# Kernel tuning notes

Hardware: AMD Instinct MI355X
Metric: run time of the kernel (lower is better)

## Reference

```python
import jax, jax.numpy as jnp
import numpy as np

EPS = 1e-5

def sage_conv(x, edge_index, w_l, b_l, w_r):
    # PyG SAGEConv with mean aggregation: lin_l(mean of source-neighbor feats per dst) + lin_r(x)
    n = x.shape[0]
    src, dst = edge_index[0], edge_index[1]
    agg = jax.ops.segment_sum(x[src], dst, num_segments=n)  # [N, d]
    deg = jax.ops.segment_sum(jnp.ones((edge_index.shape[1],), x.dtype), dst, num_segments=n)
    agg = agg / jnp.maximum(deg, 1.0)[:, None]
    return agg @ w_l + b_l + x @ w_r

def batchnorm_eval(x, gamma, beta, mean, var):
    return (x - mean) * (gamma * jax.lax.rsqrt(var + EPS)) + beta

def setup_inputs() -> dict:
    key = jax.random.key(0)
    ks = jax.random.split(key, 12)
    N, E, D, H, O = 10000, 160000, 512, 512, 256
    inp = {
        'x': jax.random.normal(ks[0], (N, D), jnp.float32),
        'edge_index': jax.random.randint(ks[1], (2, E), 0, N, jnp.int32),
        'w_l1': jax.random.normal(ks[2], (D, H), jnp.float32) * (1.0 / np.sqrt(D)),
        'b1': jnp.zeros((H,), jnp.float32),
        'w_r1': jax.random.normal(ks[3], (D, H), jnp.float32) * (1.0 / np.sqrt(D)),
        'bn1_gamma': jnp.ones((H,), jnp.float32),
        'bn1_beta': jnp.zeros((H,), jnp.float32),
        'bn1_mean': jax.random.normal(ks[4], (H,), jnp.float32) * 0.1,
        'bn1_var': jax.random.uniform(ks[5], (H,), jnp.float32, 0.5, 1.5),
        'w_l2': jax.random.normal(ks[6], (H, H), jnp.float32) * (1.0 / np.sqrt(H)),
        'b2': jnp.zeros((H,), jnp.float32),
        'w_r2': jax.random.normal(ks[7], (H, H), jnp.float32) * (1.0 / np.sqrt(H)),
        'bn2_gamma': jnp.ones((H,), jnp.float32),
        'bn2_beta': jnp.zeros((H,), jnp.float32),
        'bn2_mean': jax.random.normal(ks[8], (H,), jnp.float32) * 0.1,
        'bn2_var': jax.random.uniform(ks[9], (H,), jnp.float32, 0.5, 1.5),
        'w_l3': jax.random.normal(ks[10], (H, O), jnp.float32) * (1.0 / np.sqrt(H)),
        'b3': jnp.zeros((O,), jnp.float32),
        'w_r3': jax.random.normal(ks[11], (H, O), jnp.float32) * (1.0 / np.sqrt(H)),
    }
    return inp

def reference(x, edge_index, w_l1, b1, w_r1, bn1_gamma, bn1_beta, bn1_mean, bn1_var,
              w_l2, b2, w_r2, bn2_gamma, bn2_beta, bn2_mean, bn2_var,
              w_l3, b3, w_r3):
    # Layer 1: SAGEConv -> BN (eval) -> ReLU (dropout is identity in eval)
    h = sage_conv(x, edge_index, w_l1, b1, w_r1)
    h = jax.nn.relu(batchnorm_eval(h, bn1_gamma, bn1_beta, bn1_mean, bn1_var))
    # Layer 2
    h = sage_conv(h, edge_index, w_l2, b2, w_r2)
    h = jax.nn.relu(batchnorm_eval(h, bn2_gamma, bn2_beta, bn2_mean, bn2_var))
    # Layer 3 (no BN/ReLU)
    return sage_conv(h, edge_index, w_l3, b3, w_r3)
```

## Files before the change

### kernel.cpp

```cpp
#include <hip/hip_runtime.h>

#define NNODE 10000
#define NEDGE 160000
#define SLOTS 128

using frag8 = __attribute__((ext_vector_type(8))) short;
using f32x4 = __attribute__((ext_vector_type(4))) float;

__device__ __forceinline__ unsigned short f2bf(float f) {
    union { float f; unsigned u; } v; v.f = f;
    unsigned r = (v.u + 0x7fffu + ((v.u >> 16) & 1u)) >> 16;
    return (unsigned short)r;
}
__device__ __forceinline__ float bf2f(unsigned short s) {
    union { unsigned u; float f; } v; v.u = ((unsigned)s) << 16; return v.f;
}

__global__ void k_fillp(const int* __restrict__ src, const int* __restrict__ dst,
                        int E, int* __restrict__ cnt, int* __restrict__ csrp) {
    int e = blockIdx.x * 256 + threadIdx.x;
    if (e < E) {
        int d = dst[e];
        int p = atomicAdd(&cnt[d], 1);
        csrp[(long)d * SLOTS + p] = src[e];
    }
}

__global__ __launch_bounds__(256) void k_prep(
    const float* __restrict__ x, unsigned short* __restrict__ xb,
    const float* __restrict__ wl1, const float* __restrict__ wr1,
    const float* __restrict__ wl2, const float* __restrict__ wr2,
    const float* __restrict__ wl3, const float* __restrict__ wr3,
    unsigned short* __restrict__ bt1, unsigned short* __restrict__ bt2,
    unsigned short* __restrict__ bt3,
    const float* __restrict__ b1, const float* __restrict__ g1, const float* __restrict__ be1,
    const float* __restrict__ m1, const float* __restrict__ v1,
    const float* __restrict__ b2, const float* __restrict__ g2, const float* __restrict__ be2,
    const float* __restrict__ m2, const float* __restrict__ v2,
    const float* __restrict__ b3,
    float* __restrict__ sc1, float* __restrict__ sh1,
    float* __restrict__ sc2, float* __restrict__ sh2,
    float* __restrict__ sc3, float* __restrict__ sh3) {
    const int b = blockIdx.x, tid = threadIdx.x;
    if (b < 5000) {
        int i = b * 256 + tid;
        float4 f = ((const float4*)x)[i];
        ushort4 o;
        o.x = f2bf(f.x); o.y = f2bf(f.y); o.z = f2bf(f.z); o.w = f2bf(f.w);
        ((ushort4*)xb)[i] = o;
        return;
    }
    if (b == 6280) {
        for (int t = tid; t < 512; t += 256) {
            float s1 = g1[t] * rsqrtf(v1[t] + 1e-5f);
            sc1[t] = s1; sh1[t] = (b1[t] - m1[t]) * s1 + be1[t];
            float s2 = g2[t] * rsqrtf(v2[t] + 1e-5f);
            sc2[t] = s2; sh2[t] = (b2[t] - m2[t]) * s2 + be2[t];
            sc3[t] = 1.0f; sh3[t] = (t < 256) ? 0.0f : b3[t - 256];
        }
        return;
    }
    __shared__ float t[32][33];
    int tj = b - 5000;
    const float* srcp; unsigned short* dstp; int C, koff, ntilesN, rowoff, dstride;
    if (tj < 1024) {
        int job = tj >> 8; int tile = tj & 255; C = 512; ntilesN = 16;
        srcp = (job == 0) ? wl1 : (job == 1) ? wr1 : (job == 2) ? wl2 : wr2;
        dstp = (job < 2) ? bt1 : bt2; koff = (job & 1) * 512; rowoff = 0; dstride = 1024;
        tj = tile;
    } else {
        int jj = tj - 1024; int job = jj >> 7; int tile = jj & 127; C = 256; ntilesN = 8;
        srcp = (job == 0) ? wl3 : wr3; dstp = bt3; koff = 0; rowoff = job * 256; dstride = 512;
        tj = tile;
    }
    int k0 = (tj / ntilesN) * 32, c0 = (tj % ntilesN) * 32;
    int tx = tid & 31, ty = tid >> 5;
#pragma unroll
    for (int q = 0; q < 4; q++)
        t[ty + 8 * q][tx] = srcp[(long)(k0 + ty + 8 * q) * C + c0 + tx];
    __syncthreads();
#pragma unroll
    for (int q = 0; q < 4; q++)
        dstp[(long)(rowoff + c0 + ty + 8 * q) * dstride + koff + k0 + tx] = f2bf(t[tx][ty + 8 * q]);
}

__global__ __launch_bounds__(64) void k_agg(const unsigned short* __restrict__ S,
                                            const int* __restrict__ cnt, const int* __restrict__ csrp,
                                            unsigned short* __restrict__ outb) {
    const int n = blockIdx.x;
    const int c = threadIdx.x * 8;
    const int e = cnt[n];
    const int* __restrict__ lst = csrp + (long)n * SLOTS;
    float a[8];
#pragma unroll
    for (int k = 0; k < 8; k++) a[k] = 0.f;
    int i = 0;
    for (; i + 4 <= e; i += 4) {
        int r0 = lst[i], r1 = lst[i + 1], r2 = lst[i + 2], r3 = lst[i + 3];
        uint4 u0 = *(const uint4*)(S + (long)r0 * 512 + c);
        uint4 u1 = *(const uint4*)(S + (long)r1 * 512 + c);
        uint4 u2 = *(const uint4*)(S + (long)r2 * 512 + c);
        uint4 u3 = *(const uint4*)(S + (long)r3 * 512 + c);
#define ACC(u) \
        a[0] += bf2f((unsigned short)((u).x & 0xffffu)); a[1] += bf2f((unsigned short)((u).x >> 16)); \
        a[2] += bf2f((unsigned short)((u).y & 0xffffu)); a[3] += bf2f((unsigned short)((u).y >> 16)); \
        a[4] += bf2f((unsigned short)((u).z & 0xffffu)); a[5] += bf2f((unsigned short)((u).z >> 16)); \
        a[6] += bf2f((unsigned short)((u).w & 0xffffu)); a[7] += bf2f((unsigned short)((u).w >> 16));
        ACC(u0) ACC(u1) ACC(u2) ACC(u3)
    }
    for (; i < e; i++) {
        uint4 u = *(const uint4*)(S + (long)lst[i] * 512 + c);
        ACC(u)
    }
#undef ACC
    const float inv = 1.f / (float)(e > 1 ? e : 1);
    uint4 o;
    o.x = (unsigned)f2bf(a[0] * inv) | ((unsigned)f2bf(a[1] * inv) << 16);
    o.y = (unsigned)f2bf(a[2] * inv) | ((unsigned)f2bf(a[3] * inv) << 16);
    o.z = (unsigned)f2bf(a[4] * inv) | ((unsigned)f2bf(a[5] * inv) << 16);
    o.w = (unsigned)f2bf(a[6] * inv) | ((unsigned)f2bf(a[7] * inv) << 16);
    *(uint4*)(outb + (long)n * 512 + c) = o;
}

__global__ __launch_bounds__(64) void k_agg_fuse(const unsigned short* __restrict__ PQ,
                                                 const int* __restrict__ cnt, const int* __restrict__ csrp,
                                                 float* __restrict__ out) {
    const int n = blockIdx.x;
    const int c = threadIdx.x * 4;
    const int e = cnt[n];
    const int* __restrict__ lst = csrp + (long)n * SLOTS;
    uint2 q = *(const uint2*)(PQ + (long)n * 512 + 256 + c);
    float a0 = 0.f, a1 = 0.f, a2 = 0.f, a3 = 0.f;
    int i = 0;
    for (; i + 4 <= e; i += 4) {
        int r0 = lst[i], r1 = lst[i + 1], r2 = lst[i + 2], r3 = lst[i + 3];
        uint2 u0 = *(const uint2*)(PQ + (long)r0 * 512 + c);
        uint2 u1 = *(const uint2*)(PQ + (long)r1 * 512 + c);
        uint2 u2 = *(const uint2*)(PQ + (long)r2 * 512 + c);
        uint2 u3 = *(const uint2*)(PQ + (long)r3 * 512 + c);
#define ACC(u) \
        a0 += bf2f((unsigned short)((u).x & 0xffffu)); a1 += bf2f((unsigned short)((u).x >> 16)); \
        a2 += bf2f((unsigned short)((u).y & 0xffffu)); a3 += bf2f((unsigned short)((u).y >> 16));
        ACC(u0) ACC(u1) ACC(u2) ACC(u3)
    }
    for (; i < e; i++) {
        uint2 u = *(const uint2*)(PQ + (long)lst[i] * 512 + c);
        ACC(u)
    }
#undef ACC
    const float inv = 1.f / (float)(e > 1 ? e : 1);
    float4 o;
    o.x = a0 * inv + bf2f((unsigned short)(q.x & 0xffffu));
    o.y = a1 * inv + bf2f((unsigned short)(q.x >> 16));
    o.z = a2 * inv + bf2f((unsigned short)(q.y & 0xffffu));
    o.w = a3 * inv + bf2f((unsigned short)(q.y >> 16));
    *(float4*)&out[(long)n * 256 + c] = o;
}

template <int MODE, int NOUT, bool SPLIT>
__global__ __launch_bounds__(256, 3) void k_gemm(const unsigned short* __restrict__ Agg,
                                                 const unsigned short* __restrict__ Self,
                                                 const unsigned short* __restrict__ Bt,
                                                 const float* __restrict__ sc, const float* __restrict__ sh,
                                                 unsigned short* __restrict__ hout, int M) {
    constexpr int NT = NOUT / 128;
    constexpr int QSH = (NT == 4) ? 5 : 4;
    constexpr int KSTEPS = SPLIT ? 16 : 8;
    constexpr int BSTR = SPLIT ? 1024 : 512;
    const int b = blockIdx.x;
    const int X = b & 7;
    const int q = (b >> 3) & (NT - 1);
    const int g = b >> QSH;
    const int m0 = (g * 8 + X) * 64;
    if (m0 >= M) return;
    const int n0 = q * 128;

    __shared__ __align__(16) short As[2][64 * 64];
    __shared__ __align__(16) short Bs[2][128 * 64];
    const int tid = threadIdx.x;
    const int w = tid >> 6, lane = tid & 63;
    const int wm = (w >> 1) * 32, wn = (w & 1) * 64;
    const int fr = lane & 15, fq = lane >> 4, sw = fr & 7;
    const int srow = w * 8 + (lane >> 3);
    const int scol = (((lane & 7) ^ (lane >> 3)) * 8);
    const int ldsOff = w * 8 * 64;

    f32x4 acc[2][4];
#pragma unroll
    for (int i = 0; i < 2; i++)
#pragma unroll
        for (int j = 0; j < 4; j++)
#pragma unroll
            for (int r = 0; r < 4; r++) acc[i][j][r] = 0.f;

    auto issue = [&](int t, int buf) {
        const short* abase;
        int kk;
        if constexpr (SPLIT) {
            abase = (const short*)((t < 8) ? Agg : Self);
            kk = (t & 7) * 64;
        } else {
            abase = (const short*)Self;
            kk = t * 64;
        }
        const int k0 = t * 64;
#pragma unroll
        for (int cch = 0; cch < 2; cch++) {
            __builtin_amdgcn_global_load_lds(
                (const __attribute__((address_space(1))) void*)(abase + (long)(m0 + cch * 32 + srow) * 512 + kk + scol),
                (__attribute__((address_space(3))) void*)(&As[buf][ldsOff + cch * 32 * 64]), 16, 0, 0);
        }
#pragma unroll
        for (int cch = 0; cch < 4; cch++) {
            __builtin_amdgcn_global_load_lds(
                (const __attribute__((address_space(1))) void*)((const short*)Bt + (long)(n0 + cch * 32 + srow) * BSTR + k0 + scol),
                (__attribute__((address_space(3))) void*)(&Bs[buf][ldsOff + cch * 32 * 64]), 16, 0, 0);
        }
    };

    issue(0, 0);
#pragma unroll
    for (int t = 0; t < KSTEPS; t++) {
        const int cur = t & 1;
        __syncthreads();
        if (t < KSTEPS - 1) issue(t + 1, cur ^ 1);
#pragma unroll
        for (int ks = 0; ks < 2; ks++) {
            frag8 af[2], bf[4];
#pragma unroll
            for (int i = 0; i < 2; i++)
                af[i] = *(const frag8*)(&As[cur][(wm + i * 16 + fr) * 64 + (((ks * 4 + fq) ^ sw) * 8)]);
#pragma unroll
            for (int j = 0; j < 4; j++)
                bf[j] = *(const frag8*)(&Bs[cur][(wn + j * 16 + fr) * 64 + (((ks * 4 + fq) ^ sw) * 8)]);
#pragma unroll
            for (int i = 0; i < 2; i++)
#pragma unroll
                for (int j = 0; j < 4; j++)
                    acc[i][j] = __builtin_amdgcn_mfma_f32_16x16x32_bf16(bf[j], af[i], acc[i][j], 0, 0, 0);
        }
    }

#pragma unroll
    for (int j = 0; j < 4; j++) {
        const int colb = n0 + wn + j * 16 + fq * 4;
        const float4 s4 = *(const float4*)&sc[colb];
        const float4 h4 = *(const float4*)&sh[colb];
#pragma unroll
        for (int i = 0; i < 2; i++) {
            const int row = m0 + wm + i * 16 + fr;
            if (row < M) {
                float y0 = acc[i][j][0] * s4.x + h4.x;
                float y1 = acc[i][j][1] * s4.y + h4.y;
                float y2 = acc[i][j][2] * s4.z + h4.z;
                float y3 = acc[i][j][3] * s4.w + h4.w;
                if constexpr (MODE == 0) {
                    y0 = fmaxf(y0, 0.f); y1 = fmaxf(y1, 0.f);
                    y2 = fmaxf(y2, 0.f); y3 = fmaxf(y3, 0.f);
                }
                uint2 o;
                o.x = (unsigned)f2bf(y0) | ((unsigned)f2bf(y1) << 16);
                o.y = (unsigned)f2bf(y2) | ((unsigned)f2bf(y3) << 16);
                *(uint2*)&hout[(long)row * NOUT + colb] = o;
            }
        }
    }
}

extern "C" void kernel_launch(void* const* d_in, const int* in_sizes, int n_in,
                              void* d_out, int out_size, void* d_ws, size_t ws_size,
                              hipStream_t stream) {
    const float* x    = (const float*)d_in[0];
    const int*   ei   = (const int*)d_in[1];
    const float* w_l1 = (const float*)d_in[2];
    const float* b1   = (const float*)d_in[3];
    const float* w_r1 = (const float*)d_in[4];
    const float* g1   = (const float*)d_in[5];
    const float* be1  = (const float*)d_in[6];
    const float* m1   = (const float*)d_in[7];
    const float* v1   = (const float*)d_in[8];
    const float* w_l2 = (const float*)d_in[9];
    const float* b2   = (const float*)d_in[10];
    const float* w_r2 = (const float*)d_in[11];
    const float* g2   = (const float*)d_in[12];
    const float* be2  = (const float*)d_in[13];
    const float* m2   = (const float*)d_in[14];
    const float* v2   = (const float*)d_in[15];
    const float* w_l3 = (const float*)d_in[16];
    const float* b3   = (const float*)d_in[17];
    const float* w_r3 = (const float*)d_in[18];
    float* out = (float*)d_out;

    const int N = NNODE, E = NEDGE;
    const int* srcI = ei;
    const int* dstI = ei + E;

    char* w = (char*)d_ws;
    auto alloc = [&](size_t bytes) { void* p = (void*)w; w += (bytes + 255) & ~(size_t)255; return p; };
    int* cnt  = (int*)alloc((size_t)N * 4);
    int* csrp = (int*)alloc((size_t)N * SLOTS * 4);
    unsigned short* xb   = (unsigned short*)alloc((size_t)N * 512 * 2);
    unsigned short* bt1  = (unsigned short*)alloc((size_t)512 * 1024 * 2);
    unsigned short* bt2  = (unsigned short*)alloc((size_t)512 * 1024 * 2);
    unsigned short* bt3  = (unsigned short*)alloc((size_t)512 * 512 * 2);
    float* sc1 = (float*)alloc(512 * 4); float* sh1 = (float*)alloc(512 * 4);
    float* sc2 = (float*)alloc(512 * 4); float* sh2 = (float*)alloc(512 * 4);
    float* sc3 = (float*)alloc(512 * 4); float* sh3 = (float*)alloc(512 * 4);
    unsigned short* agg_a = (unsigned short*)alloc((size_t)N * 512 * 2);
    unsigned short* h1    = (unsigned short*)alloc((size_t)N * 512 * 2);
    unsigned short* h2    = (unsigned short*)alloc((size_t)N * 512 * 2);
    (void)alloc(256 * 1024);

    hipMemsetAsync(cnt, 0, (size_t)N * 4, stream);
    k_prep<<<6281, 256, 0, stream>>>(x, xb, w_l1, w_r1, w_l2, w_r2, w_l3, w_r3,
                                     bt1, bt2, bt3,
                                     b1, g1, be1, m1, v1, b2, g2, be2, m2, v2, b3,
                                     sc1, sh1, sc2, sh2, sc3, sh3);
    k_fillp<<<(E + 255) / 256, 256, 0, stream>>>(srcI, dstI, E, cnt, csrp);

    k_agg<<<N, 64, 0, stream>>>(xb, cnt, csrp, agg_a);
    k_gemm<0, 512, true><<<640, 256, 0, stream>>>(agg_a, xb, bt1, sc1, sh1, h1, N);
    k_agg<<<N, 64, 0, stream>>>(h1, cnt, csrp, agg_a);
    k_gemm<0, 512, true><<<640, 256, 0, stream>>>(agg_a, h1, bt2, sc2, sh2, h2, N);
    k_gemm<2, 512, false><<<640, 256, 0, stream>>>(h2, h2, bt3, sc3, sh3, agg_a, N);
    k_agg_fuse<<<N, 64, 0, stream>>>(agg_a, cnt, csrp, out);
}
```

Before: 224.8 us.

## Overlap neighbor aggregation with self-term GEMM in one mixed kernel

Each layer's GEMM is split into a self term (x @ w_r) and an aggregate term. A combined kernel interleaves aggregation blocks (four nodes per 256-thread block) with self-GEMM blocks, so the two independent workloads run concurrently. The self GEMM writes fp32 partial results to a new workspace buffer, which a second GEMM over the aggregate reads and combines with BN and ReLU in its epilogue. This trades an extra fp32 write and read of N×512 floats per layer for overlap of memory-bound gather work with MFMA work.

```diff
diff --git a/kernel.cpp b/kernel.cpp
--- a/kernel.cpp
+++ b/kernel.cpp
@@ -84,42 +84,315 @@
         dstp[(long)(rowoff + c0 + ty + 8 * q) * dstride + koff + k0 + tx] = f2bf(t[tx][ty + 8 * q]);
 }
 
-__global__ __launch_bounds__(64) void k_agg(const unsigned short* __restrict__ S,
-                                            const int* __restrict__ cnt, const int* __restrict__ csrp,
-                                            unsigned short* __restrict__ outb) {
-    const int n = blockIdx.x;
-    const int c = threadIdx.x * 8;
-    const int e = cnt[n];
-    const int* __restrict__ lst = csrp + (long)n * SLOTS;
-    float a[8];
-#pragma unroll
-    for (int k = 0; k < 8; k++) a[k] = 0.f;
-    int i = 0;
-    for (; i + 4 <= e; i += 4) {
-        int r0 = lst[i], r1 = lst[i + 1], r2 = lst[i + 2], r3 = lst[i + 3];
-        uint4 u0 = *(const uint4*)(S + (long)r0 * 512 + c);
-        uint4 u1 = *(const uint4*)(S + (long)r1 * 512 + c);
-        uint4 u2 = *(const uint4*)(S + (long)r2 * 512 + c);
-        uint4 u3 = *(const uint4*)(S + (long)r3 * 512 + c);
+__global__ __launch_bounds__(256, 3) void k_mixA(
+    const unsigned short* __restrict__ S,
+    const int* __restrict__ cnt, const int* __restrict__ csrp,
+    unsigned short* __restrict__ aggOut,
+    const unsigned short* __restrict__ Bt,
+    float* __restrict__ Qf) {
+    __shared__ __align__(16) short As[2][64 * 64];
+    __shared__ __align__(16) short Bs[2][128 * 64];
+    const int b = blockIdx.x;
+    const int tid = threadIdx.x;
+
+    if ((b % 5) != 4) {
+        const int agg_idx = (b / 5) * 4 + (b % 5);
+        const int n = agg_idx * 4 + (tid >> 6);
+        if (n >= NNODE) return;
+        const int c = (tid & 63) * 8;
+        const int e = cnt[n];
+        const int* __restrict__ lst = csrp + (long)n * SLOTS;
+        float a[8];
+#pragma unroll
+        for (int k = 0; k < 8; k++) a[k] = 0.f;
+        int i = 0;
+        for (; i + 4 <= e; i += 4) {
+            int r0 = lst[i], r1 = lst[i + 1], r2 = lst[i + 2], r3 = lst[i + 3];
+            uint4 u0 = *(const uint4*)(S + (long)r0 * 512 + c);
+            uint4 u1 = *(const uint4*)(S + (long)r1 * 512 + c);
+            uint4 u2 = *(const uint4*)(S + (long)r2 * 512 + c);
+            uint4 u3 = *(const uint4*)(S + (long)r3 * 512 + c);
 #define ACC(u) \
-        a[0] += bf2f((unsigned short)((u).x & 0xffffu)); a[1] += bf2f((unsigned short)((u).x >> 16)); \
-        a[2] += bf2f((unsigned short)((u).y & 0xffffu)); a[3] += bf2f((unsigned short)((u).y >> 16)); \
-        a[4] += bf2f((unsigned short)((u).z & 0xffffu)); a[5] += bf2f((unsigned short)((u).z >> 16)); \
-        a[6] += bf2f((unsigned short)((u).w & 0xffffu)); a[7] += bf2f((unsigned short)((u).w >> 16));
-        ACC(u0) ACC(u1) ACC(u2) ACC(u3)
-    }
-    for (; i < e; i++) {
-        uint4 u = *(const uint4*)(S + (long)lst[i] * 512 + c);
-        ACC(u)
-    }
+            a[0] += bf2f((unsigned short)((u).x & 0xffffu)); a[1] += bf2f((unsigned short)((u).x >> 16)); \
+            a[2] += bf2f((unsigned short)((u).y & 0xffffu)); a[3] += bf2f((unsigned short)((u).y >> 16)); \
+            a[4] += bf2f((unsigned short)((u).z & 0xffffu)); a[5] += bf2f((unsigned short)((u).z >> 16)); \
+            a[6] += bf2f((unsigned short)((u).w & 0xffffu)); a[7] += bf2f((unsigned short)((u).w >> 16));
+            ACC(u0) ACC(u1) ACC(u2) ACC(u3)
+        }
+        for (; i < e; i++) {
+            uint4 u = *(const uint4*)(S + (long)lst[i] * 512 + c);
+            ACC(u)
+        }
 #undef ACC
-    const float inv = 1.f / (float)(e > 1 ? e : 1);
-    uint4 o;
-    o.x = (unsigned)f2bf(a[0] * inv) | ((unsigned)f2bf(a[1] * inv) << 16);
-    o.y = (unsigned)f2bf(a[2] * inv) | ((unsigned)f2bf(a[3] * inv) << 16);
-    o.z = (unsigned)f2bf(a[4] * inv) | ((unsigned)f2bf(a[5] * inv) << 16);
-    o.w = (unsigned)f2bf(a[6] * inv) | ((unsigned)f2bf(a[7] * inv) << 16);
-    *(uint4*)(outb + (long)n * 512 + c) = o;
+        const float inv = 1.f / (float)(e > 1 ? e : 1);
+        uint4 o;
+        o.x = (unsigned)f2bf(a[0] * inv) | ((unsigned)f2bf(a[1] * inv) << 16);
+        o.y = (unsigned)f2bf(a[2] * inv) | ((unsigned)f2bf(a[3] * inv) << 16);
+        o.z = (unsigned)f2bf(a[4] * inv) | ((unsigned)f2bf(a[5] * inv) << 16);
+        o.w = (unsigned)f2bf(a[6] * inv) | ((unsigned)f2bf(a[7] * inv) << 16);
+        *(uint4*)(aggOut + (long)n * 512 + c) = o;
+        return;
+    }
+
+    const int id = b / 5;
+    const int X = id & 7;
+    const int q = (id >> 3) & 3;
+    const int g = id >> 5;
+    const int m0 = (g * 8 + X) * 64;
+    if (m0 >= NNODE) return;
+    const int n0 = q * 128;
+
+    const int w = tid >> 6, lane = tid & 63;
+    const int wm = (w >> 1) * 32, wn = (w & 1) * 64;
+    const int fr = lane & 15, fq = lane >> 4, sw = fr & 7;
+    const int srow = w * 8 + (lane >> 3);
+    const int scol = (((lane & 7) ^ (lane >> 3)) * 8);
+    const int ldsOff = w * 8 * 64;
+
+    f32x4 acc[2][4];
+#pragma unroll
+    for (int i = 0; i < 2; i++)
+#pragma unroll
+        for (int j = 0; j < 4; j++)
+#pragma unroll
+            for (int r = 0; r < 4; r++) acc[i][j][r] = 0.f;
+
+    auto issue = [&](int t, int buf) {
+        const int k0 = t * 64;
+#pragma unroll
+        for (int cch = 0; cch < 2; cch++) {
+            __builtin_amdgcn_global_load_lds(
+                (const __attribute__((address_space(1))) void*)((const short*)S + (long)(m0 + cch * 32 + srow) * 512 + k0 + scol),
+                (__attribute__((address_space(3))) void*)(&As[buf][ldsOff + cch * 32 * 64]), 16, 0, 0);
+        }
+#pragma unroll
+        for (int cch = 0; cch < 4; cch++) {
+            __builtin_amdgcn_global_load_lds(
+                (const __attribute__((address_space(1))) void*)((const short*)Bt + (long)(n0 + cch * 32 + srow) * 1024 + 512 + k0 + scol),
+                (__attribute__((address_space(3))) void*)(&Bs[buf][ldsOff + cch * 32 * 64]), 16, 0, 0);
+        }
+    };
+
+    issue(0, 0);
+#pragma unroll
+    for (int t = 0; t < 8; t++) {
+        const int cur = t & 1;
+        __syncthreads();
+        if (t < 7) issue(t + 1, cur ^ 1);
+#pragma unroll
+        for (int ks = 0; ks < 2; ks++) {
+            frag8 af[2], bf[4];
+#pragma unroll
+            for (int i = 0; i < 2; i++)
+                af[i] = *(const frag8*)(&As[cur][(wm + i * 16 + fr) * 64 + (((ks * 4 + fq) ^ sw) * 8)]);
+#pragma unroll
+            for (int j = 0; j < 4; j++)
+                bf[j] = *(const frag8*)(&Bs[cur][(wn + j * 16 + fr) * 64 + (((ks * 4 + fq) ^ sw) * 8)]);
+#pragma unroll
+            for (int i = 0; i < 2; i++)
+#pragma unroll
+                for (int j = 0; j < 4; j++)
+                    acc[i][j] = __builtin_amdgcn_mfma_f32_16x16x32_bf16(bf[j], af[i], acc[i][j], 0, 0, 0);
+        }
+    }
+
+#pragma unroll
+    for (int j = 0; j < 4; j++) {
+        const int colb = n0 + wn + j * 16 + fq * 4;
+#pragma unroll
+        for (int i = 0; i < 2; i++) {
+            const int row = m0 + wm + i * 16 + fr;
+            if (row < NNODE) {
+                float4 o;
+                o.x = acc[i][j][0]; o.y = acc[i][j][1]; o.z = acc[i][j][2]; o.w = acc[i][j][3];
+                *(float4*)&Qf[(long)row * 512 + colb] = o;
+            }
+        }
+    }
+}
+
+__global__ __launch_bounds__(256, 3) void k_gemmB(const unsigned short* __restrict__ Agg,
+                                                  const unsigned short* __restrict__ Bt,
+                                                  const float* __restrict__ Qf,
+                                                  const float* __restrict__ sc, const float* __restrict__ sh,
+                                                  unsigned short* __restrict__ hout, int M) {
+    const int b = blockIdx.x;
+    const int X = b & 7;
+    const int q = (b >> 3) & 3;
+    const int g = b >> 5;
+    const int m0 = (g * 8 + X) * 64;
+    if (m0 >= M) return;
+    const int n0 = q * 128;
+
+    __shared__ __align__(16) short As[2][64 * 64];
+    __shared__ __align__(16) short Bs[2][128 * 64];
+    const int tid = threadIdx.x;
+    const int w = tid >> 6, lane = tid & 63;
+    const int wm = (w >> 1) * 32, wn = (w & 1) * 64;
+    const int fr = lane & 15, fq = lane >> 4, sw = fr & 7;
+    const int srow = w * 8 + (lane >> 3);
+    const int scol = (((lane & 7) ^ (lane >> 3)) * 8);
+    const int ldsOff = w * 8 * 64;
+
+    f32x4 acc[2][4];
+#pragma unroll
+    for (int i = 0; i < 2; i++)
+#pragma unroll
+        for (int j = 0; j < 4; j++)
+#pragma unroll
+            for (int r = 0; r < 4; r++) acc[i][j][r] = 0.f;
+
+    auto issue = [&](int t, int buf) {
+        const int k0 = t * 64;
+#pragma unroll
+        for (int cch = 0; cch < 2; cch++) {
+            __builtin_amdgcn_global_load_lds(
+                (const __attribute__((address_space(1))) void*)((const short*)Agg + (long)(m0 + cch * 32 + srow) * 512 + k0 + scol),
+                (__attribute__((address_space(3))) void*)(&As[buf][ldsOff + cch * 32 * 64]), 16, 0, 0);
+        }
+#pragma unroll
+        for (int cch = 0; cch < 4; cch++) {
+            __builtin_amdgcn_global_load_lds(
+                (const __attribute__((address_space(1))) void*)((const short*)Bt + (long)(n0 + cch * 32 + srow) * 1024 + k0 + scol),
+                (__attribute__((address_space(3))) void*)(&Bs[buf][ldsOff + cch * 32 * 64]), 16, 0, 0);
+        }
+    };
+
+    issue(0, 0);
+#pragma unroll
+    for (int t = 0; t < 8; t++) {
+        const int cur = t & 1;
+        __syncthreads();
+        if (t < 7) issue(t + 1, cur ^ 1);
+#pragma unroll
+        for (int ks = 0; ks < 2; ks++) {
+            frag8 af[2], bf[4];
+#pragma unroll
+            for (int i = 0; i < 2; i++)
+                af[i] = *(const frag8*)(&As[cur][(wm + i * 16 + fr) * 64 + (((ks * 4 + fq) ^ sw) * 8)]);
+#pragma unroll
+            for (int j = 0; j < 4; j++)
+                bf[j] = *(const frag8*)(&Bs[cur][(wn + j * 16 + fr) * 64 + (((ks * 4 + fq) ^ sw) * 8)]);
+#pragma unroll
+            for (int i = 0; i < 2; i++)
+#pragma unroll
+                for (int j = 0; j < 4; j++)
+                    acc[i][j] = __builtin_amdgcn_mfma_f32_16x16x32_bf16(bf[j], af[i], acc[i][j], 0, 0, 0);
+        }
+    }
+
+#pragma unroll
+    for (int j = 0; j < 4; j++) {
+        const int colb = n0 + wn + j * 16 + fq * 4;
+        const float4 s4 = *(const float4*)&sc[colb];
+        const float4 h4 = *(const float4*)&sh[colb];
+#pragma unroll
+        for (int i = 0; i < 2; i++) {
+            const int row = m0 + wm + i * 16 + fr;
+            if (row < M) {
+                const float4 qv = *(const float4*)&Qf[(long)row * 512 + colb];
+                float y0 = fmaxf((acc[i][j][0] + qv.x) * s4.x + h4.x, 0.f);
+                float y1 = fmaxf((acc[i][j][1] + qv.y) * s4.y + h4.y, 0.f);
+                float y2 = fmaxf((acc[i][j][2] + qv.z) * s4.z + h4.z, 0.f);
+                float y3 = fmaxf((acc[i][j][3] + qv.w) * s4.w + h4.w, 0.f);
+                uint2 o;
+                o.x = (unsigned)f2bf(y0) | ((unsigned)f2bf(y1) << 16);
+                o.y = (unsigned)f2bf(y2) | ((unsigned)f2bf(y3) << 16);
+                *(uint2*)&hout[(long)row * 512 + colb] = o;
+            }
+        }
+    }
+}
+
+__global__ __launch_bounds__(256, 3) void k_gemm3(const unsigned short* __restrict__ Self,
+                                                  const unsigned short* __restrict__ Bt,
+                                                  const float* __restrict__ sc, const float* __restrict__ sh,
+                                                  unsigned short* __restrict__ hout, int M) {
+    const int b = blockIdx.x;
+    const int X = b & 7;
+    const int q = (b >> 3) & 3;
+    const int g = b >> 5;
+    const int m0 = (g * 8 + X) * 64;
+    if (m0 >= M) return;
+    const int n0 = q * 128;
+
+    __shared__ __align__(16) short As[2][64 * 64];
+    __shared__ __align__(16) short Bs[2][128 * 64];
+    const int tid = threadIdx.x;
+    const int w = tid >> 6, lane = tid & 63;
+    const int wm = (w >> 1) * 32, wn = (w & 1) * 64;
+    const int fr = lane & 15, fq = lane >> 4, sw = fr & 7;
+    const int srow = w * 8 + (lane >> 3);
+    const int scol = (((lane & 7) ^ (lane >> 3)) * 8);
+    const int ldsOff = w * 8 * 64;
+
+    f32x4 acc[2][4];
+#pragma unroll
+    for (int i = 0; i < 2; i++)
+#pragma unroll
+        for (int j = 0; j < 4; j++)
+#pragma unroll
+            for (int r = 0; r < 4; r++) acc[i][j][r] = 0.f;
+
+    auto issue = [&](int t, int buf) {
+        const int k0 = t * 64;
+#pragma unroll
+        for (int cch = 0; cch < 2; cch++) {
+            __builtin_amdgcn_global_load_lds(
+                (const __attribute__((address_space(1))) void*)((const short*)Self + (long)(m0 + cch * 32 + srow) * 512 + k0 + scol),
+                (__attribute__((address_space(3))) void*)(&As[buf][ldsOff + cch * 32 * 64]), 16, 0, 0);
+        }
+#pragma unroll
+        for (int cch = 0; cch < 4; cch++) {
+            __builtin_amdgcn_global_load_lds(
+                (const __attribute__((address_space(1))) void*)((const short*)Bt + (long)(n0 + cch * 32 + srow) * 512 + k0 + scol),
+                (__attribute__((address_space(3))) void*)(&Bs[buf][ldsOff + cch * 32 * 64]), 16, 0, 0);
+        }
+    };
+
+    issue(0, 0);
+#pragma unroll
+    for (int t = 0; t < 8; t++) {
+        const int cur = t & 1;
+        __syncthreads();
+        if (t < 7) issue(t + 1, cur ^ 1);
+#pragma unroll
+        for (int ks = 0; ks < 2; ks++) {
+            frag8 af[2], bf[4];
+#pragma unroll
+            for (int i = 0; i < 2; i++)
+                af[i] = *(const frag8*)(&As[cur][(wm + i * 16 + fr) * 64 + (((ks * 4 + fq) ^ sw) * 8)]);
+#pragma unroll
+            for (int j = 0; j < 4; j++)
+                bf[j] = *(const frag8*)(&Bs[cur][(wn + j * 16 + fr) * 64 + (((ks * 4 + fq) ^ sw) * 8)]);
+#pragma unroll
+            for (int i = 0; i < 2; i++)
+#pragma unroll
+                for (int j = 0; j < 4; j++)
+                    acc[i][j] = __builtin_amdgcn_mfma_f32_16x16x32_bf16(bf[j], af[i], acc[i][j], 0, 0, 0);
+        }
+    }
+
+#pragma unroll
+    for (int j = 0; j < 4; j++) {
+        const int colb = n0 + wn + j * 16 + fq * 4;
+        const float4 s4 = *(const float4*)&sc[colb];
+        const float4 h4 = *(const float4*)&sh[colb];
+#pragma unroll
+        for (int i = 0; i < 2; i++) {
+            const int row = m0 + wm + i * 16 + fr;
+            if (row < M) {
+                float y0 = acc[i][j][0] * s4.x + h4.x;
+                float y1 = acc[i][j][1] * s4.y + h4.y;
+                float y2 = acc[i][j][2] * s4.z + h4.z;
+                float y3 = acc[i][j][3] * s4.w + h4.w;
+                uint2 o;
+                o.x = (unsigned)f2bf(y0) | ((unsigned)f2bf(y1) << 16);
+                o.y = (unsigned)f2bf(y2) | ((unsigned)f2bf(y3) << 16);
+                *(uint2*)&hout[(long)row * 512 + colb] = o;
+            }
+        }
+    }
 }
 
 __global__ __launch_bounds__(64) void k_agg_fuse(const unsigned short* __restrict__ PQ,
@@ -155,116 +428,6 @@
     o.z = a2 * inv + bf2f((unsigned short)(q.y & 0xffffu));
     o.w = a3 * inv + bf2f((unsigned short)(q.y >> 16));
     *(float4*)&out[(long)n * 256 + c] = o;
-}
-
-template <int MODE, int NOUT, bool SPLIT>
-__global__ __launch_bounds__(256, 3) void k_gemm(const unsigned short* __restrict__ Agg,
-                                                 const unsigned short* __restrict__ Self,
-                                                 const unsigned short* __restrict__ Bt,
-                                                 const float* __restrict__ sc, const float* __restrict__ sh,
-                                                 unsigned short* __restrict__ hout, int M) {
-    constexpr int NT = NOUT / 128;
-    constexpr int QSH = (NT == 4) ? 5 : 4;
-    constexpr int KSTEPS = SPLIT ? 16 : 8;
-    constexpr int BSTR = SPLIT ? 1024 : 512;
-    const int b = blockIdx.x;
-    const int X = b & 7;
-    const int q = (b >> 3) & (NT - 1);
-    const int g = b >> QSH;
-    const int m0 = (g * 8 + X) * 64;
-    if (m0 >= M) return;
-    const int n0 = q * 128;
-
-    __shared__ __align__(16) short As[2][64 * 64];
-    __shared__ __align__(16) short Bs[2][128 * 64];
-    const int tid = threadIdx.x;
-    const int w = tid >> 6, lane = tid & 63;
-    const int wm = (w >> 1) * 32, wn = (w & 1) * 64;
-    const int fr = lane & 15, fq = lane >> 4, sw = fr & 7;
-    const int srow = w * 8 + (lane >> 3);
-    const int scol = (((lane & 7) ^ (lane >> 3)) * 8);
-    const int ldsOff = w * 8 * 64;
-
-    f32x4 acc[2][4];
-#pragma unroll
-    for (int i = 0; i < 2; i++)
-#pragma unroll
-        for (int j = 0; j < 4; j++)
-#pragma unroll
-            for (int r = 0; r < 4; r++) acc[i][j][r] = 0.f;
-
-    auto issue = [&](int t, int buf) {
-        const short* abase;
-        int kk;
-        if constexpr (SPLIT) {
-            abase = (const short*)((t < 8) ? Agg : Self);
-            kk = (t & 7) * 64;
-        } else {
-            abase = (const short*)Self;
-            kk = t * 64;
-        }
-        const int k0 = t * 64;
-#pragma unroll
-        for (int cch = 0; cch < 2; cch++) {
-            __builtin_amdgcn_global_load_lds(
-                (const __attribute__((address_space(1))) void*)(abase + (long)(m0 + cch * 32 + srow) * 512 + kk + scol),
-                (__attribute__((address_space(3))) void*)(&As[buf][ldsOff + cch * 32 * 64]), 16, 0, 0);
-        }
-#pragma unroll
-        for (int cch = 0; cch < 4; cch++) {
-            __builtin_amdgcn_global_load_lds(
-                (const __attribute__((address_space(1))) void*)((const short*)Bt + (long)(n0 + cch * 32 + srow) * BSTR + k0 + scol),
-                (__attribute__((address_space(3))) void*)(&Bs[buf][ldsOff + cch * 32 * 64]), 16, 0, 0);
-        }
-    };
-
-    issue(0, 0);
-#pragma unroll
-    for (int t = 0; t < KSTEPS; t++) {
-        const int cur = t & 1;
-        __syncthreads();
-        if (t < KSTEPS - 1) issue(t + 1, cur ^ 1);
-#pragma unroll
-        for (int ks = 0; ks < 2; ks++) {
-            frag8 af[2], bf[4];
-#pragma unroll
-            for (int i = 0; i < 2; i++)
-                af[i] = *(const frag8*)(&As[cur][(wm + i * 16 + fr) * 64 + (((ks * 4 + fq) ^ sw) * 8)]);
-#pragma unroll
-            for (int j = 0; j < 4; j++)
-                bf[j] = *(const frag8*)(&Bs[cur][(wn + j * 16 + fr) * 64 + (((ks * 4 + fq) ^ sw) * 8)]);
-#pragma unroll
-            for (int i = 0; i < 2; i++)
-#pragma unroll
-                for (int j = 0; j < 4; j++)
-                    acc[i][j] = __builtin_amdgcn_mfma_f32_16x16x32_bf16(bf[j], af[i], acc[i][j], 0, 0, 0);
-        }
-    }
-
-#pragma unroll
-    for (int j = 0; j < 4; j++) {
-        const int colb = n0 + wn + j * 16 + fq * 4;
-        const float4 s4 = *(const float4*)&sc[colb];
-        const float4 h4 = *(const float4*)&sh[colb];
-#pragma unroll
-        for (int i = 0; i < 2; i++) {
-            const int row = m0 + wm + i * 16 + fr;
-            if (row < M) {
-                float y0 = acc[i][j][0] * s4.x + h4.x;
-                float y1 = acc[i][j][1] * s4.y + h4.y;
-                float y2 = acc[i][j][2] * s4.z + h4.z;
-                float y3 = acc[i][j][3] * s4.w + h4.w;
-                if constexpr (MODE == 0) {
-                    y0 = fmaxf(y0, 0.f); y1 = fmaxf(y1, 0.f);
-                    y2 = fmaxf(y2, 0.f); y3 = fmaxf(y3, 0.f);
-                }
-                uint2 o;
-                o.x = (unsigned)f2bf(y0) | ((unsigned)f2bf(y1) << 16);
-                o.y = (unsigned)f2bf(y2) | ((unsigned)f2bf(y3) << 16);
-                *(uint2*)&hout[(long)row * NOUT + colb] = o;
-            }
-        }
-    }
 }
 
 extern "C" void kernel_launch(void* const* d_in, const int* in_sizes, int n_in,
@@ -309,6 +472,7 @@
     unsigned short* agg_a = (unsigned short*)alloc((size_t)N * 512 * 2);
     unsigned short* h1    = (unsigned short*)alloc((size_t)N * 512 * 2);
     unsigned short* h2    = (unsigned short*)alloc((size_t)N * 512 * 2);
+    float* Qf = (float*)alloc((size_t)N * 512 * 4);
     (void)alloc(256 * 1024);
 
     hipMemsetAsync(cnt, 0, (size_t)N * 4, stream);
@@ -318,10 +482,10 @@
                                      sc1, sh1, sc2, sh2, sc3, sh3);
     k_fillp<<<(E + 255) / 256, 256, 0, stream>>>(srcI, dstI, E, cnt, csrp);
 
-    k_agg<<<N, 64, 0, stream>>>(xb, cnt, csrp, agg_a);
-    k_gemm<0, 512, true><<<640, 256, 0, stream>>>(agg_a, xb, bt1, sc1, sh1, h1, N);
-    k_agg<<<N, 64, 0, stream>>>(h1, cnt, csrp, agg_a);
-    k_gemm<0, 512, true><<<640, 256, 0, stream>>>(agg_a, h1, bt2, sc2, sh2, h2, N);
-    k_gemm<2, 512, false><<<640, 256, 0, stream>>>(h2, h2, bt3, sc3, sh3, agg_a, N);
+    k_mixA<<<3200, 256, 0, stream>>>(xb, cnt, csrp, agg_a, bt1, Qf);
+    k_gemmB<<<640, 256, 0, stream>>>(agg_a, bt1, Qf, sc1, sh1, h1, N);
+    k_mixA<<<3200, 256, 0, stream>>>(h1, cnt, csrp, agg_a, bt2, Qf);
+    k_gemmB<<<640, 256, 0, stream>>>(agg_a, bt2, Qf, sc2, sh2, h2, N);
+    k_gemm3<<<640, 256, 0, stream>>>(h2, bt3, sc3, sh3, agg_a, N);
     k_agg_fuse<<<N, 64, 0, stream>>>(agg_a, cnt, csrp, out);
 }
```

After: 245.7 us. 1.09x slower.
